# Optimization experiments

Measured on AMD Instinct MI355X. Metric: run time of the kernel, lower is better.

Reference implementation:

```python
import jax, jax.numpy as jnp
import numpy as np

B, C_IN, L = 4, 128, 2048
HEADS, C_HEAD = 8, 32
HIDDEN = HEADS * C_HEAD  # 256
EPS = 1e-5


def setup_inputs() -> dict:
    key = jax.random.key(0)
    ks = jax.random.split(key, 6)
    return {
        "x": jax.random.normal(ks[0], (B, C_IN, L), dtype=jnp.float32),
        "w_qkv": jax.random.normal(ks[1], (3 * HIDDEN, C_IN), dtype=jnp.float32) * 0.05,
        "b_qkv": jax.random.normal(ks[2], (3 * HIDDEN,), dtype=jnp.float32) * 0.05,
        "w_out": jax.random.normal(ks[3], (C_IN, HIDDEN), dtype=jnp.float32) * 0.05,
        "b_out": jax.random.normal(ks[4], (C_IN,), dtype=jnp.float32) * 0.05,
        "bn_weight": jnp.ones((C_IN,), dtype=jnp.float32),
        "bn_bias": jnp.zeros((C_IN,), dtype=jnp.float32),
        "bn_mean": jnp.zeros((C_IN,), dtype=jnp.float32),
        "bn_var": jnp.ones((C_IN,), dtype=jnp.float32),
    }


def reference(x, w_qkv, b_qkv, w_out, b_out, bn_weight, bn_bias, bn_mean, bn_var):
    # 1x1 conv == channel matmul: (B, 3*hidden, L)
    qkv = jnp.einsum('oi,bil->bol', w_qkv, x) + b_qkv[None, :, None]
    # '(qkv heads c) l -> qkv heads l c' (batched)
    qkv = qkv.reshape(B, 3, HEADS, C_HEAD, L).transpose(1, 0, 2, 4, 3)  # (3,B,H,L,c)
    q, k, v = qkv[0], qkv[1], qkv[2]
    # Faithful quirk: original scales q by sqrt(q.shape[1]) == sqrt(L), not sqrt(c)
    q = q / jnp.sqrt(jnp.float32(L))
    # scores (B,H,L,L), softmax over last axis
    scores = jnp.einsum('bhqd,bhkd->bhqk', q, k)
    ctx = jax.nn.softmax(scores, axis=-1)
    # Faithful quirk: 'hca,hcb->hab' contracts over the QUERY axis of ctx
    attn = jnp.einsum('bhqa,bhqd->bhad', ctx, v)  # (B,H,L,c)
    # 'heads l h -> (heads h) l'
    attn = attn.transpose(0, 1, 3, 2).reshape(B, HIDDEN, L)
    out = jnp.einsum('oi,bil->bol', w_out, attn) + b_out[None, :, None]
    out = out + x
    # BatchNorm inference mode with running stats, per-channel
    inv = bn_weight / jnp.sqrt(bn_var + EPS)
    out = out * inv[None, :, None] + (bn_bias - bn_mean * inv)[None, :, None]
    return out
```

## Files before the change

### kernel.cpp

```cpp
#include <hip/hip_runtime.h>
#include <math.h>

#define BB 4
#define CIN 128
#define LL 2048
#define HH 8
#define CH 32
#define HID 256

typedef __attribute__((ext_vector_type(8))) __bf16 bf16x8;
typedef __attribute__((ext_vector_type(4))) float f32x4;
typedef __attribute__((ext_vector_type(16))) float f32x16;

static __device__ __forceinline__ unsigned int f2bf(float f) {
    union { __bf16 b; unsigned short s; } u;
    u.b = (__bf16)f;
    return (unsigned int)u.s;
}
static __device__ __forceinline__ float bf2f(unsigned int s) {
    union { float f; unsigned int u; } x;
    x.u = s << 16;
    return x.f;
}

#define MFMA   __builtin_amdgcn_mfma_f32_16x16x32_bf16
#define MFMA32 __builtin_amdgcn_mfma_f32_32x32x16_bf16
#define E2(x)  __builtin_amdgcn_exp2f(x)

__global__ __launch_bounds__(256) void qkv_mfma(
        const float* __restrict__ x, const float* __restrict__ w_qkv,
        const float* __restrict__ b_qkv,
        unsigned short* __restrict__ qb, unsigned short* __restrict__ kb,
        unsigned short* __restrict__ vtb) {
    __shared__ float tr2[128][66];
    __shared__ unsigned short wlds2[32][136];
    __shared__ float tr[32 * 65];
    const int t = threadIdx.x, w = t >> 6, lane = t & 63;
    const int r = lane & 15, gq = lane >> 4;
    const int lt = blockIdx.x;
    const int h  = blockIdx.y;
    const int b  = blockIdx.z;
    const int l0 = lt * 64;

    {
        const int ll = t & 63, ig = t >> 6;
        const float* xp = x + (size_t)b * CIN * LL + l0 + ll;
        #pragma unroll
        for (int k = 0; k < 32; ++k) {
            const int i = k * 4 + ig;
            tr2[i][ll] = xp[(size_t)i * LL];
        }
    }
    __syncthreads();

    bf16x8 bfr[4];
    #pragma unroll
    for (int ks = 0; ks < 4; ++ks) {
        union { uint4 u; bf16x8 v; } p;
        const int i0 = gq * 8 + ks * 32, lx = w * 16 + r;
        p.u.x = f2bf(tr2[i0 + 0][lx]) | (f2bf(tr2[i0 + 1][lx]) << 16);
        p.u.y = f2bf(tr2[i0 + 2][lx]) | (f2bf(tr2[i0 + 3][lx]) << 16);
        p.u.z = f2bf(tr2[i0 + 4][lx]) | (f2bf(tr2[i0 + 5][lx]) << 16);
        p.u.w = f2bf(tr2[i0 + 6][lx]) | (f2bf(tr2[i0 + 7][lx]) << 16);
        bfr[ks] = p.v;
    }

    for (int sel = 0; sel < 3; ++sel) {
        const int obase = sel * 256 + h * 32;
        __syncthreads();
        #pragma unroll
        for (int k2 = 0; k2 < 2; ++k2) {
            int idx = t + k2 * 256;
            int row = idx >> 4, col8 = (idx & 15) * 8;
            const float* wsrc = w_qkv + (size_t)(obase + row) * CIN + col8;
            float4 a4 = *(const float4*)(wsrc);
            float4 b4 = *(const float4*)(wsrc + 4);
            uint4 o;
            o.x = f2bf(a4.x) | (f2bf(a4.y) << 16);
            o.y = f2bf(a4.z) | (f2bf(a4.w) << 16);
            o.z = f2bf(b4.x) | (f2bf(b4.y) << 16);
            o.w = f2bf(b4.z) | (f2bf(b4.w) << 16);
            *(uint4*)&wlds2[row][col8] = o;
        }
        __syncthreads();

        f32x4 acc0 = {0,0,0,0}, acc1 = {0,0,0,0};
        #pragma unroll
        for (int ks = 0; ks < 4; ++ks) {
            bf16x8 a0 = *(const bf16x8*)&wlds2[r][gq * 8 + ks * 32];
            bf16x8 a1 = *(const bf16x8*)&wlds2[16 + r][gq * 8 + ks * 32];
            acc0 = MFMA(a0, bfr[ks], acc0, 0, 0, 0);
            acc1 = MFMA(a1, bfr[ks], acc1, 0, 0, 0);
        }
        const float scale = (sel == 0) ? 0.03187935835f : 1.0f;
        #pragma unroll
        for (int reg = 0; reg < 4; ++reg) {
            const int oc0 = gq * 4 + reg;
            tr[oc0 * 65 + w * 16 + r] = (acc0[reg] + b_qkv[obase + oc0]) * scale;
            const int oc1 = 16 + gq * 4 + reg;
            tr[oc1 * 65 + w * 16 + r] = (acc1[reg] + b_qkv[obase + oc1]) * scale;
        }
        __syncthreads();

        if (sel == 2) {
            unsigned short* dst = vtb + ((size_t)(b * HH + h) * CH) * LL + l0;
            #pragma unroll
            for (int rr = 0; rr < 8; ++rr) {
                int flat = rr * 256 + t;
                int c = flat >> 6, l = flat & 63;
                dst[(size_t)c * LL + l] = (unsigned short)f2bf(tr[c * 65 + l]);
            }
        } else {
            unsigned short* dst = (sel == 0 ? qb : kb)
                                  + ((size_t)(b * HH + h) * LL + l0) * CH;
            #pragma unroll
            for (int rr = 0; rr < 8; ++rr) {
                int flat = rr * 256 + t;
                int c = flat & 31, lr = flat >> 5;
                dst[flat] = (unsigned short)f2bf(tr[c * 65 + lr]);
            }
        }
    }
}

__global__ __launch_bounds__(512, 4) void denom_mfma(
        const unsigned short* __restrict__ qb,
        const unsigned short* __restrict__ kb,
        unsigned short* __restrict__ vtb) {
    __shared__ unsigned short klds[2][256][40];
    __shared__ float zz[128];
    const int t = threadIdx.x, wave = t >> 6, lane = t & 63;
    const int id = blockIdx.x;
    const int bh = (id & 7) * 4 + (id >> 7);
    const int qt = (id >> 3) & 15;
    const int r = lane & 15, g = lane >> 4;
    const int q0 = qt * 128 + wave * 16;

    bf16x8 afrag = *(const bf16x8*)(qb + ((size_t)bh * LL + q0 + r) * CH + 8 * g);

    const unsigned short* kbase = kb + (size_t)bh * LL * CH;

    float z0 = 0.f, z1 = 0.f, z2 = 0.f, z3 = 0.f;
    const f32x4 zero = {0.f, 0.f, 0.f, 0.f};

    #pragma unroll
    for (int k2 = 0; k2 < 2; ++k2) {
        int ts2 = t + 512 * k2;
        int a = ts2 >> 2, dcol = (ts2 & 3) * 8;
        *(uint4*)(&klds[0][0][0] + a * 40 + dcol) =
            *(const uint4*)(kbase + (size_t)a * CH + dcol);
    }
    __syncthreads();

    const int rb = r * 40 + 8 * g;
    for (int c = 0; c < 8; ++c) {
        const int cur = c & 1;
        uint4 nreg0, nreg1;
        if (c < 7) {
            int ts0 = t, ts1 = t + 512;
            nreg0 = *(const uint4*)(kbase + (size_t)((c + 1) * 256 + (ts0 >> 2)) * CH
                                    + (ts0 & 3) * 8);
            nreg1 = *(const uint4*)(kbase + (size_t)((c + 1) * 256 + (ts1 >> 2)) * CH
                                    + (ts1 & 3) * 8);
        }
        const unsigned short* kc = &klds[cur][0][0];
        #pragma unroll
        for (int s = 0; s < 16; ++s) {
            bf16x8 bf = *(const bf16x8*)(kc + s * 16 * 40 + rb);
            f32x4 d = MFMA(afrag, bf, zero, 0, 0, 0);
            z0 += E2(d[0]); z1 += E2(d[1]); z2 += E2(d[2]); z3 += E2(d[3]);
        }
        if (c < 7) {
            unsigned short* kd = &klds[cur ^ 1][0][0];
            int ts0 = t, ts1 = t + 512;
            *(uint4*)(kd + (ts0 >> 2) * 40 + (ts0 & 3) * 8) = nreg0;
            *(uint4*)(kd + (ts1 >> 2) * 40 + (ts1 & 3) * 8) = nreg1;
        }
        __syncthreads();
    }

    #pragma unroll
    for (int m = 1; m < 16; m <<= 1) {
        z0 += __shfl_xor(z0, m); z1 += __shfl_xor(z1, m);
        z2 += __shfl_xor(z2, m); z3 += __shfl_xor(z3, m);
    }
    if (r == 0)
        *(float4*)&zz[wave * 16 + 4 * g] = make_float4(z0, z1, z2, z3);
    __syncthreads();
    if (t < 128) zz[t] = 1.0f / zz[t];
    __syncthreads();

    const int d = t >> 4, qo = (t & 15) * 8;
    unsigned short* vrow = vtb + ((size_t)bh * CH + d) * LL + qt * 128 + qo;
    uint4 v = *(const uint4*)vrow;
    const float* zp = &zz[qo];
    unsigned int w0, w1, w2, w3;
    w0 = f2bf(bf2f(v.x & 0xFFFFu) * zp[0]) | (f2bf(bf2f(v.x >> 16) * zp[1]) << 16);
    w1 = f2bf(bf2f(v.y & 0xFFFFu) * zp[2]) | (f2bf(bf2f(v.y >> 16) * zp[3]) << 16);
    w2 = f2bf(bf2f(v.z & 0xFFFFu) * zp[4]) | (f2bf(bf2f(v.z >> 16) * zp[5]) << 16);
    w3 = f2bf(bf2f(v.w & 0xFFFFu) * zp[6]) | (f2bf(bf2f(v.w >> 16) * zp[7]) << 16);
    *(uint4*)vrow = make_uint4(w0, w1, w2, w3);
}

__global__ __launch_bounds__(512, 4) void attn_mfma(
        const unsigned short* __restrict__ qb,
        const unsigned short* __restrict__ kb,
        const unsigned short* __restrict__ vtb,
        float* __restrict__ attnT) {
    __shared__ unsigned short qlds[2][128][40];
    __shared__ unsigned short vlds[2][128][40];
    const int t = threadIdx.x, wave = t >> 6, lane = t & 63;
    const int ln = lane & 31, hi = lane >> 5;
    const int id = blockIdx.x;
    const int bhqh = (id & 7) * 8 + (id >> 6);
    const int at = (id >> 3) & 7;
    const int bh = bhqh >> 1, qh = bhqh & 1;
    const int b = bh >> 3, h = bh & 7;
    const int a0 = at * 256 + wave * 32;
    const int q00 = qh * 1024;

    const unsigned short* kp = kb + ((size_t)bh * LL + a0 + ln) * CH + 8 * hi;
    const bf16x8 kf0 = *(const bf16x8*)kp;
    const bf16x8 kf1 = *(const bf16x8*)(kp + 16);

    unsigned short* const ql0 = &qlds[0][0][0];
    unsigned short* const ql1 = &qlds[1][0][0];
    unsigned short* const vl0 = &vlds[0][0][0];
    unsigned short* const vl1 = &vlds[1][0][0];

    const int ts = t & 255;
    int sq[2], sv[2];
    const unsigned short *qsa[2], *vsa[2];
    #pragma unroll
    for (int k2 = 0; k2 < 2; ++k2) {
        int ts2 = ts + 256 * k2;
        int q = ts2 >> 2, dcol = (ts2 & 3) * 8;
        qsa[k2] = qb + ((size_t)bh * LL + q00 + q) * CH + dcol;
        sq[k2] = q * 40 + dcol;
        int sub = ts2 >> 7, vd = (ts2 >> 2) & 31, vq = (ts2 & 3) * 8;
        vsa[k2] = vtb + ((size_t)bh * CH + vd) * LL + q00 + sub * 32 + vq;
        sv[k2] = (sub * 32 + vd) * 40 + vq;
    }

    f32x16 acc = {0.f,0.f,0.f,0.f,0.f,0.f,0.f,0.f,0.f,0.f,0.f,0.f,0.f,0.f,0.f,0.f};
    const f32x16 zero16 = {0.f,0.f,0.f,0.f,0.f,0.f,0.f,0.f,0.f,0.f,0.f,0.f,0.f,0.f,0.f,0.f};

#define CVTPK(dst, lo_, hi_) \
    asm("v_cvt_pk_bf16_f32 %0, %1, %2" : "=v"(dst) : "v"(lo_), "v"(hi_))
#define SWAPH(a_, b_) \
    asm("v_permlane32_swap_b32 %0, %1" : "+v"(a_), "+v"(b_))

    #pragma unroll
    for (int k2 = 0; k2 < 2; ++k2) {
        if (wave < 4) *(uint4*)(ql0 + sq[k2]) = *(const uint4*)(qsa[k2]);
        else          *(uint4*)(vl0 + sv[k2]) = *(const uint4*)(vsa[k2]);
    }
    __syncthreads();

    for (int n = 0; n < 8; ++n) {
        const int cur = n & 1;
        uint4 nreg0, nreg1;
        if (n < 7) {
            if (wave < 4) {
                nreg0 = *(const uint4*)(qsa[0] + (size_t)(n + 1) * 128 * CH);
                nreg1 = *(const uint4*)(qsa[1] + (size_t)(n + 1) * 128 * CH);
            } else {
                nreg0 = *(const uint4*)(vsa[0] + (n + 1) * 128);
                nreg1 = *(const uint4*)(vsa[1] + (n + 1) * 128);
            }
        }
        const unsigned short* qc = cur ? ql1 : ql0;
        const unsigned short* vc = cur ? vl1 : vl0;
        #pragma unroll
        for (int s2 = 0; s2 < 4; ++s2) {
            const int rdq = (s2 * 32 + ln) * 40 + 8 * hi;
            bf16x8 qa0 = *(const bf16x8*)(qc + rdq);
            bf16x8 qa1 = *(const bf16x8*)(qc + rdq + 16);
            bf16x8 vb0 = *(const bf16x8*)(vc + rdq);
            bf16x8 vb1 = *(const bf16x8*)(vc + rdq + 16);
            f32x16 s = MFMA32(qa0, kf0, zero16, 0, 0, 0);
            s = MFMA32(qa1, kf1, s, 0, 0, 0);
            unsigned int w0, w1, w2, w3, w4, w5, w6, w7;
            {
                float p0  = E2(s[0]),  p1  = E2(s[1]),  p2  = E2(s[2]),  p3  = E2(s[3]);
                float p4  = E2(s[4]),  p5  = E2(s[5]),  p6  = E2(s[6]),  p7  = E2(s[7]);
                float p8  = E2(s[8]),  p9  = E2(s[9]),  p10 = E2(s[10]), p11 = E2(s[11]);
                float p12 = E2(s[12]), p13 = E2(s[13]), p14 = E2(s[14]), p15 = E2(s[15]);
                CVTPK(w0, p0,  p1);  CVTPK(w1, p2,  p3);
                CVTPK(w2, p4,  p5);  CVTPK(w3, p6,  p7);
                CVTPK(w4, p8,  p9);  CVTPK(w5, p10, p11);
                CVTPK(w6, p12, p13); CVTPK(w7, p14, p15);
                SWAPH(w0, w2); SWAPH(w1, w3); SWAPH(w4, w6); SWAPH(w5, w7);
            }
            union { uint4 u; bf16x8 v; } pa0, pa1;
            pa0.u = make_uint4(w0, w1, w2, w3);
            pa1.u = make_uint4(w4, w5, w6, w7);
            __builtin_amdgcn_s_setprio(1);
            acc = MFMA32(pa0.v, vb0, acc, 0, 0, 0);
            acc = MFMA32(pa1.v, vb1, acc, 0, 0, 0);
            __builtin_amdgcn_s_setprio(0);
        }
        if (n < 7) {
            unsigned short* qd = cur ? ql0 : ql1;
            unsigned short* vd = cur ? vl0 : vl1;
            if (wave < 4) {
                *(uint4*)(qd + sq[0]) = nreg0;
                *(uint4*)(qd + sq[1]) = nreg1;
            } else {
                *(uint4*)(vd + sv[0]) = nreg0;
                *(uint4*)(vd + sv[1]) = nreg1;
            }
        }
        __syncthreads();
    }

#undef SWAPH
#undef CVTPK

    float* ob = attnT + ((size_t)qh * BB * HID + (size_t)b * HID + h * CH + ln) * LL
                + a0 + 4 * hi;
    *(f32x4*)(ob +  0) = __builtin_shufflevector(acc, acc,  0,  1,  2,  3);
    *(f32x4*)(ob +  8) = __builtin_shufflevector(acc, acc,  4,  5,  6,  7);
    *(f32x4*)(ob + 16) = __builtin_shufflevector(acc, acc,  8,  9, 10, 11);
    *(f32x4*)(ob + 24) = __builtin_shufflevector(acc, acc, 12, 13, 14, 15);
}

__global__ __launch_bounds__(256, 4) void out_mfma(
        const float* __restrict__ attnT, const float* __restrict__ w_out,
        const float* __restrict__ x, const float* __restrict__ b_out,
        const float* __restrict__ bnw, const float* __restrict__ bnb,
        const float* __restrict__ bnm, const float* __restrict__ bnv,
        float* __restrict__ out) {
    __shared__ unsigned short alds[2][32][40];
    __shared__ unsigned short wlds[2][128][40];
    const int t = threadIdx.x, wave = t >> 6, lane = t & 63;
    const int ln = lane & 31, hi = lane >> 5;
    const int id = blockIdx.x;
    const int bid = (id & 7) * 32 + (id >> 3);
    const int b = bid >> 6, lt = bid & 63;
    const int l0 = lt * 32;
    const size_t PART = (size_t)BB * HID * LL;
    const int WBUF = 128 * 40;

    const int si = t >> 3, sl4 = (t & 7) * 4;
    const float* ap0 = attnT + ((size_t)b * HID + si) * LL + l0 + sl4;
    const float* wsrc0 = w_out + (size_t)(t >> 2) * HID + (t & 3) * 8;
    const float* wsrc1 = wsrc0 + (size_t)64 * HID;
    unsigned short* const wdst0 = &wlds[0][t >> 2][(t & 3) * 8];

    f32x16 acc = {0.f,0.f,0.f,0.f,0.f,0.f,0.f,0.f,0.f,0.f,0.f,0.f,0.f,0.f,0.f,0.f};

#define PACKW(dst, p) do { \
    float4 a4 = *(const float4*)(p); \
    float4 b4 = *(const float4*)((p) + 4); \
    uint4 o_; \
    o_.x = f2bf(a4.x) | (f2bf(a4.y) << 16); \
    o_.y = f2bf(a4.z) | (f2bf(a4.w) << 16); \
    o_.z = f2bf(b4.x) | (f2bf(b4.y) << 16); \
    o_.w = f2bf(b4.z) | (f2bf(b4.w) << 16); \
    *(uint4*)(dst) = o_; \
} while (0)

    {
        f32x4 a0 = *(const f32x4*)(ap0);
        f32x4 a1 = *(const f32x4*)(ap0 + PART);
        #pragma unroll
        for (int j = 0; j < 4; ++j)
            alds[0][sl4 + j][si] = (unsigned short)f2bf(a0[j] + a1[j]);
        PACKW(wdst0, wsrc0);
        PACKW(wdst0 + 64 * 40, wsrc1);
    }
    __syncthreads();

    for (int c = 0; c < 8; ++c) {
        const int cur = c & 1;
        f32x4 na0, na1;
        if (c < 7) {
            na0 = *(const f32x4*)(ap0 + (size_t)(c + 1) * 32 * LL);
            na1 = *(const f32x4*)(ap0 + (size_t)(c + 1) * 32 * LL + PART);
        }
        const unsigned short* wc = &wlds[cur][0][0] + (wave * 32 + ln) * 40 + 8 * hi;
        const unsigned short* ac = &alds[cur][0][0] + ln * 40 + 8 * hi;
        bf16x8 af0 = *(const bf16x8*)(wc);
        bf16x8 af1 = *(const bf16x8*)(wc + 16);
        bf16x8 bf0 = *(const bf16x8*)(ac);
        bf16x8 bf1 = *(const bf16x8*)(ac + 16);
        acc = MFMA32(af0, bf0, acc, 0, 0, 0);
        acc = MFMA32(af1, bf1, acc, 0, 0, 0);
        if (c < 7) {
            const int nb = cur ^ 1;
            #pragma unroll
            for (int j = 0; j < 4; ++j)
                alds[nb][sl4 + j][si] = (unsigned short)f2bf(na0[j] + na1[j]);
            PACKW(wdst0 + nb * WBUF, wsrc0 + (c + 1) * 32);
            PACKW(wdst0 + nb * WBUF + 64 * 40, wsrc1 + (c + 1) * 32);
        }
        __syncthreads();
    }
#undef PACKW

    #pragma unroll
    for (int reg = 0; reg < 16; ++reg) {
        const int o = wave * 32 + (reg & 3) + 8 * (reg >> 2) + 4 * hi;
        const float inv = bnw[o] / sqrtf(bnv[o] + 1e-5f);
        const float sh  = bnb[o] - bnm[o] * inv;
        const size_t idx = ((size_t)b * CIN + o) * LL + l0 + ln;
        float val = acc[reg] + b_out[o] + x[idx];
        out[idx] = val * inv + sh;
    }
}

extern "C" void kernel_launch(void* const* d_in, const int* in_sizes, int n_in,
                              void* d_out, int out_size, void* d_ws, size_t ws_size,
                              hipStream_t stream) {
    const float* x      = (const float*)d_in[0];
    const float* w_qkv  = (const float*)d_in[1];
    const float* b_qkv  = (const float*)d_in[2];
    const float* w_out  = (const float*)d_in[3];
    const float* b_out  = (const float*)d_in[4];
    const float* bnw    = (const float*)d_in[5];
    const float* bnb    = (const float*)d_in[6];
    const float* bnm    = (const float*)d_in[7];
    const float* bnv    = (const float*)d_in[8];
    float* out = (float*)d_out;

    const size_t NBH = (size_t)BB * HH;
    const size_t QKV_ELEMS = NBH * LL * CH;
    unsigned short* qb    = (unsigned short*)d_ws;
    unsigned short* kb    = qb + QKV_ELEMS;
    unsigned short* vtb   = kb + QKV_ELEMS;
    float* attnT = (float*)(vtb + QKV_ELEMS);

    qkv_mfma<<<dim3(32, 8, BB), 256, 0, stream>>>(x, w_qkv, b_qkv, qb, kb, vtb);
    denom_mfma<<<dim3(512), 512, 0, stream>>>(qb, kb, vtb);
    attn_mfma<<<dim3(512), 512, 0, stream>>>(qb, kb, vtb, attnT);
    out_mfma<<<dim3(256), 256, 0, stream>>>(attnT, w_out, x, b_out,
                                            bnw, bnb, bnm, bnv, out);
}
```

Measured before the change: 70.33 us.

## Split out-projection over output-channel halves and K halves with LDS reduction

The output projection kernel now launches 512 blocks instead of 256. Each block covers 64 output channels instead of 128, and the four waves split as two output tiles times two K halves. The K halves are reduced through shared memory before the bias, residual and batchnorm epilogue. The goal is more parallelism and a shorter serial K loop (4 iterations instead of 8) in a small kernel that underfills the GPU. In exchange, each attnT tile is read twice across blocks, and the kernel adds an extra LDS reduction and barrier.

```diff
diff --git a/kernel.cpp b/kernel.cpp
--- a/kernel.cpp
+++ b/kernel.cpp
@@ -331,82 +331,121 @@
         const float* __restrict__ bnw, const float* __restrict__ bnb,
         const float* __restrict__ bnm, const float* __restrict__ bnv,
         float* __restrict__ out) {
-    __shared__ unsigned short alds[2][32][40];
-    __shared__ unsigned short wlds[2][128][40];
+    __shared__ unsigned short alds[2][2][32][40];
+    __shared__ unsigned short wlds[2][2][64][40];
+    __shared__ float red[2][32][33];
     const int t = threadIdx.x, wave = t >> 6, lane = t & 63;
     const int ln = lane & 31, hi = lane >> 5;
+    const int otile = wave >> 1, khalf = wave & 1;
     const int id = blockIdx.x;
-    const int bid = (id & 7) * 32 + (id >> 3);
-    const int b = bid >> 6, lt = bid & 63;
+    const int bid = (id & 7) * 64 + (id >> 3);
+    const int b = bid >> 7;
+    const int rest = bid & 127;
+    const int lt = rest >> 1, oh = rest & 1;
     const int l0 = lt * 32;
+    const int obase = oh * 64;
     const size_t PART = (size_t)BB * HID * LL;
-    const int WBUF = 128 * 40;
-
-    const int si = t >> 3, sl4 = (t & 7) * 4;
-    const float* ap0 = attnT + ((size_t)b * HID + si) * LL + l0 + sl4;
-    const float* wsrc0 = w_out + (size_t)(t >> 2) * HID + (t & 3) * 8;
-    const float* wsrc1 = wsrc0 + (size_t)64 * HID;
-    unsigned short* const wdst0 = &wlds[0][t >> 2][(t & 3) * 8];
+
+    const int as = t >> 7, ai = (t & 127) >> 2, al8 = (t & 3) * 8;
+    const float* apb = attnT + ((size_t)b * HID + as * 128 + ai) * LL + l0 + al8;
+    const int ws = t >> 7, wrow = (t & 127) >> 1, wcolg = (t & 1) * 16;
+    const float* wpb = w_out + (size_t)(obase + wrow) * HID + ws * 128 + wcolg;
 
     f32x16 acc = {0.f,0.f,0.f,0.f,0.f,0.f,0.f,0.f,0.f,0.f,0.f,0.f,0.f,0.f,0.f,0.f};
 
-#define PACKW(dst, p) do { \
-    float4 a4 = *(const float4*)(p); \
-    float4 b4 = *(const float4*)((p) + 4); \
-    uint4 o_; \
-    o_.x = f2bf(a4.x) | (f2bf(a4.y) << 16); \
-    o_.y = f2bf(a4.z) | (f2bf(a4.w) << 16); \
-    o_.z = f2bf(b4.x) | (f2bf(b4.y) << 16); \
-    o_.w = f2bf(b4.z) | (f2bf(b4.w) << 16); \
-    *(uint4*)(dst) = o_; \
-} while (0)
-
     {
-        f32x4 a0 = *(const f32x4*)(ap0);
-        f32x4 a1 = *(const f32x4*)(ap0 + PART);
-        #pragma unroll
-        for (int j = 0; j < 4; ++j)
-            alds[0][sl4 + j][si] = (unsigned short)f2bf(a0[j] + a1[j]);
-        PACKW(wdst0, wsrc0);
-        PACKW(wdst0 + 64 * 40, wsrc1);
-    }
-    __syncthreads();
-
-    for (int c = 0; c < 8; ++c) {
+        f32x4 a0 = *(const f32x4*)(apb);
+        f32x4 a0b = *(const f32x4*)(apb + 4);
+        f32x4 a1 = *(const f32x4*)(apb + PART);
+        f32x4 a1b = *(const f32x4*)(apb + PART + 4);
+        #pragma unroll
+        for (int j = 0; j < 4; ++j) {
+            alds[0][as][al8 + j][ai]     = (unsigned short)f2bf(a0[j] + a1[j]);
+            alds[0][as][al8 + 4 + j][ai] = (unsigned short)f2bf(a0b[j] + a1b[j]);
+        }
+        float4 wa = *(const float4*)(wpb);
+        float4 wb2 = *(const float4*)(wpb + 4);
+        float4 wc = *(const float4*)(wpb + 8);
+        float4 wd = *(const float4*)(wpb + 12);
+        uint4 o_;
+        o_.x = f2bf(wa.x) | (f2bf(wa.y) << 16);
+        o_.y = f2bf(wa.z) | (f2bf(wa.w) << 16);
+        o_.z = f2bf(wb2.x) | (f2bf(wb2.y) << 16);
+        o_.w = f2bf(wb2.z) | (f2bf(wb2.w) << 16);
+        *(uint4*)&wlds[0][ws][wrow][wcolg] = o_;
+        o_.x = f2bf(wc.x) | (f2bf(wc.y) << 16);
+        o_.y = f2bf(wc.z) | (f2bf(wc.w) << 16);
+        o_.z = f2bf(wd.x) | (f2bf(wd.y) << 16);
+        o_.w = f2bf(wd.z) | (f2bf(wd.w) << 16);
+        *(uint4*)&wlds[0][ws][wrow][wcolg + 8] = o_;
+    }
+    __syncthreads();
+
+    for (int c = 0; c < 4; ++c) {
         const int cur = c & 1;
-        f32x4 na0, na1;
-        if (c < 7) {
-            na0 = *(const f32x4*)(ap0 + (size_t)(c + 1) * 32 * LL);
-            na1 = *(const f32x4*)(ap0 + (size_t)(c + 1) * 32 * LL + PART);
-        }
-        const unsigned short* wc = &wlds[cur][0][0] + (wave * 32 + ln) * 40 + 8 * hi;
-        const unsigned short* ac = &alds[cur][0][0] + ln * 40 + 8 * hi;
-        bf16x8 af0 = *(const bf16x8*)(wc);
-        bf16x8 af1 = *(const bf16x8*)(wc + 16);
-        bf16x8 bf0 = *(const bf16x8*)(ac);
-        bf16x8 bf1 = *(const bf16x8*)(ac + 16);
+        f32x4 na0, na0b, na1, na1b;
+        float4 nwa, nwb, nwc, nwd;
+        if (c < 3) {
+            const float* apn = apb + (size_t)(c + 1) * 32 * LL;
+            na0  = *(const f32x4*)(apn);
+            na0b = *(const f32x4*)(apn + 4);
+            na1  = *(const f32x4*)(apn + PART);
+            na1b = *(const f32x4*)(apn + PART + 4);
+            const float* wpn = wpb + (c + 1) * 32;
+            nwa = *(const float4*)(wpn);
+            nwb = *(const float4*)(wpn + 4);
+            nwc = *(const float4*)(wpn + 8);
+            nwd = *(const float4*)(wpn + 12);
+        }
+        const unsigned short* wc_ = &wlds[cur][khalf][otile * 32 + ln][8 * hi];
+        const unsigned short* ac_ = &alds[cur][khalf][ln][8 * hi];
+        bf16x8 af0 = *(const bf16x8*)(wc_);
+        bf16x8 af1 = *(const bf16x8*)(wc_ + 16);
+        bf16x8 bf0 = *(const bf16x8*)(ac_);
+        bf16x8 bf1 = *(const bf16x8*)(ac_ + 16);
         acc = MFMA32(af0, bf0, acc, 0, 0, 0);
         acc = MFMA32(af1, bf1, acc, 0, 0, 0);
-        if (c < 7) {
+        if (c < 3) {
             const int nb = cur ^ 1;
             #pragma unroll
-            for (int j = 0; j < 4; ++j)
-                alds[nb][sl4 + j][si] = (unsigned short)f2bf(na0[j] + na1[j]);
-            PACKW(wdst0 + nb * WBUF, wsrc0 + (c + 1) * 32);
-            PACKW(wdst0 + nb * WBUF + 64 * 40, wsrc1 + (c + 1) * 32);
-        }
-        __syncthreads();
-    }
-#undef PACKW
-
-    #pragma unroll
-    for (int reg = 0; reg < 16; ++reg) {
-        const int o = wave * 32 + (reg & 3) + 8 * (reg >> 2) + 4 * hi;
-        const float inv = bnw[o] / sqrtf(bnv[o] + 1e-5f);
-        const float sh  = bnb[o] - bnm[o] * inv;
-        const size_t idx = ((size_t)b * CIN + o) * LL + l0 + ln;
-        float val = acc[reg] + b_out[o] + x[idx];
-        out[idx] = val * inv + sh;
+            for (int j = 0; j < 4; ++j) {
+                alds[nb][as][al8 + j][ai]     = (unsigned short)f2bf(na0[j] + na1[j]);
+                alds[nb][as][al8 + 4 + j][ai] = (unsigned short)f2bf(na0b[j] + na1b[j]);
+            }
+            uint4 o_;
+            o_.x = f2bf(nwa.x) | (f2bf(nwa.y) << 16);
+            o_.y = f2bf(nwa.z) | (f2bf(nwa.w) << 16);
+            o_.z = f2bf(nwb.x) | (f2bf(nwb.y) << 16);
+            o_.w = f2bf(nwb.z) | (f2bf(nwb.w) << 16);
+            *(uint4*)&wlds[nb][ws][wrow][wcolg] = o_;
+            o_.x = f2bf(nwc.x) | (f2bf(nwc.y) << 16);
+            o_.y = f2bf(nwc.z) | (f2bf(nwc.w) << 16);
+            o_.z = f2bf(nwd.x) | (f2bf(nwd.y) << 16);
+            o_.w = f2bf(nwd.z) | (f2bf(nwd.w) << 16);
+            *(uint4*)&wlds[nb][ws][wrow][wcolg + 8] = o_;
+        }
+        __syncthreads();
+    }
+
+    if (khalf == 1) {
+        #pragma unroll
+        for (int reg = 0; reg < 16; ++reg) {
+            const int orow = (reg & 3) + 8 * (reg >> 2) + 4 * hi;
+            red[otile][orow][ln] = acc[reg];
+        }
+    }
+    __syncthreads();
+    if (khalf == 0) {
+        #pragma unroll
+        for (int reg = 0; reg < 16; ++reg) {
+            const int orow = (reg & 3) + 8 * (reg >> 2) + 4 * hi;
+            const int o = obase + otile * 32 + orow;
+            const float inv = bnw[o] / sqrtf(bnv[o] + 1e-5f);
+            const float sh  = bnb[o] - bnm[o] * inv;
+            const size_t idx = ((size_t)b * CIN + o) * LL + l0 + ln;
+            float val = acc[reg] + red[otile][orow][ln] + b_out[o] + x[idx];
+            out[idx] = val * inv + sh;
+        }
     }
 }
 
@@ -434,6 +473,6 @@
     qkv_mfma<<<dim3(32, 8, BB), 256, 0, stream>>>(x, w_qkv, b_qkv, qb, kb, vtb);
     denom_mfma<<<dim3(512), 512, 0, stream>>>(qb, kb, vtb);
     attn_mfma<<<dim3(512), 512, 0, stream>>>(qb, kb, vtb, attnT);
-    out_mfma<<<dim3(256), 256, 0, stream>>>(attnT, w_out, x, b_out,
+    out_mfma<<<dim3(512), 256, 0, stream>>>(attnT, w_out, x, b_out,
                                             bnw, bnb, bnm, bnv, out);
 }
```

Result: no change. 69.28 us (-1.5%).
